# Optimization experiments

Hardware: AMD Instinct MI355X
Metric: run time of the kernel (lower is better)

## Reference

```python
import jax, jax.numpy as jnp
import numpy as np

EPS = 1e-5  # nn.LayerNorm default
T, B, HID, L = 32, 256, 384, 3
E_ENT, E_SPA, E_SCA = 256, 256, 640
D_IN = E_ENT + E_SPA + E_SCA  # 1152


def layer_norm(x, g, b):
    mu = jnp.mean(x, axis=-1, keepdims=True)
    var = jnp.var(x, axis=-1, keepdims=True)
    return (x - mu) * jax.lax.rsqrt(var + EPS) * g + b


def setup_inputs() -> dict:
    key = jax.random.key(0)
    ks = jax.random.split(key, 12)
    s_in = 0.02
    return {
        "embedded_entity": jax.random.normal(ks[0], (T, B, E_ENT), jnp.float32),
        "embedded_spatial": jax.random.normal(ks[1], (T, B, E_SPA), jnp.float32),
        "embedded_scalar": jax.random.normal(ks[2], (T, B, E_SCA), jnp.float32),
        "h0": jnp.zeros((L, B, HID), jnp.float32),
        "c0": jnp.zeros((L, B, HID), jnp.float32),
        "wx0": jax.random.normal(ks[3], (D_IN, 4 * HID), jnp.float32) * s_in,
        "wx1": jax.random.normal(ks[4], (HID, 4 * HID), jnp.float32) * s_in,
        "wx2": jax.random.normal(ks[5], (HID, 4 * HID), jnp.float32) * s_in,
        "wh": jax.random.normal(ks[6], (L, HID, 4 * HID), jnp.float32) * s_in,
        "bias": jnp.zeros((L, 4 * HID), jnp.float32),
        "gxw": jnp.ones((L, 4 * HID), jnp.float32) + 0.01 * jax.random.normal(ks[7], (L, 4 * HID), jnp.float32),
        "gxb": 0.01 * jax.random.normal(ks[8], (L, 4 * HID), jnp.float32),
        "ghw": jnp.ones((L, 4 * HID), jnp.float32) + 0.01 * jax.random.normal(ks[9], (L, 4 * HID), jnp.float32),
        "ghb": 0.01 * jax.random.normal(ks[10], (L, 4 * HID), jnp.float32),
    }


def _ln_lstm(x, h0, c0, wx_list, wh, bias, gxw, gxb, ghw, ghb):
    # x: [T, B, D]; returns output [T, B, H], (H_final, C_final) each [L, B, H]
    Hs, Cs = [], []
    for l in range(wh.shape[0]):
        # LayerNorm is per-row, so the input-side projection+LN can be batched over time
        xg = layer_norm(jnp.einsum('tbd,dk->tbk', x, wx_list[l]), gxw[l], gxb[l])
        wh_l, ghw_l, ghb_l, b_l = wh[l], ghw[l], ghb[l], bias[l]

        def step(carry, xg_t):
            h, c = carry
            gate = xg_t + layer_norm(h @ wh_l, ghw_l, ghb_l) + b_l
            i, f, o, u = jnp.split(gate, 4, axis=-1)
            c = jax.nn.sigmoid(f) * c + jax.nn.sigmoid(i) * jnp.tanh(u)
            h = jax.nn.sigmoid(o) * jnp.tanh(c)
            return (h, c), h

        (h, c), x = jax.lax.scan(step, (h0[l], c0[l]), xg)
        Hs.append(h)
        Cs.append(c)
    return x, jnp.stack(Hs), jnp.stack(Cs)


def reference(embedded_entity, embedded_spatial, embedded_scalar, h0, c0,
              wx0, wx1, wx2, wh, bias, gxw, gxb, ghw, ghb):
    embedded = jnp.concatenate([embedded_entity, embedded_spatial, embedded_scalar], axis=2)
    output, Hn, Cn = _ln_lstm(embedded, h0, c0, [wx0, wx1, wx2], wh, bias, gxw, gxb, ghw, ghb)
    return output, Hn, Cn
```

## Files before the change

### kernel.cpp

```cpp
#include <hip/hip_runtime.h>
#include <math.h>

constexpr int TT = 32;
constexpr int BB = 256;
constexpr int HH = 384;
constexpr int GG = 1536;
constexpr float LN_EPS = 1e-5f;

template<bool CONCAT>
__global__ __launch_bounds__(256)
void gemm64(const float* __restrict__ A,
            const float* __restrict__ Aent, const float* __restrict__ Aspa,
            const float* __restrict__ Asca,
            const float* __restrict__ B, float* __restrict__ C,
            int M, int K, int N)
{
    __shared__ float As[16][64];
    __shared__ float Bs[16][64];
    const int tid = threadIdx.x;
    const int bm = blockIdx.y * 64;
    const int bn = blockIdx.x * 64;
    const int tr = tid >> 4;
    const int tc = tid & 15;
    const int ar = tid >> 2;
    const int ac = (tid & 3) * 4;
    const int br = tid >> 4;
    const int bc = (tid & 15) * 4;

    float acc[4][4] = {};

    for (int k0 = 0; k0 < K; k0 += 16) {
        float4 av;
        const int arow = bm + ar;
        const int acol = k0 + ac;
        if (CONCAT) {
            const float* p;
            if (acol < 256)      p = Aent + arow * 256 + acol;
            else if (acol < 512) p = Aspa + arow * 256 + (acol - 256);
            else                 p = Asca + arow * 640 + (acol - 512);
            av = *reinterpret_cast<const float4*>(p);
        } else {
            av = *reinterpret_cast<const float4*>(A + arow * (long)K + acol);
        }
        As[ac + 0][ar] = av.x;
        As[ac + 1][ar] = av.y;
        As[ac + 2][ar] = av.z;
        As[ac + 3][ar] = av.w;
        *reinterpret_cast<float4*>(&Bs[br][bc]) =
            *reinterpret_cast<const float4*>(B + (k0 + br) * (long)N + bn + bc);
        __syncthreads();
        #pragma unroll
        for (int k = 0; k < 16; ++k) {
            const float4 a = *reinterpret_cast<const float4*>(&As[k][tr * 4]);
            const float4 b = *reinterpret_cast<const float4*>(&Bs[k][tc * 4]);
            acc[0][0] += a.x * b.x; acc[0][1] += a.x * b.y; acc[0][2] += a.x * b.z; acc[0][3] += a.x * b.w;
            acc[1][0] += a.y * b.x; acc[1][1] += a.y * b.y; acc[1][2] += a.y * b.z; acc[1][3] += a.y * b.w;
            acc[2][0] += a.z * b.x; acc[2][1] += a.z * b.y; acc[2][2] += a.z * b.z; acc[2][3] += a.z * b.w;
            acc[3][0] += a.w * b.x; acc[3][1] += a.w * b.y; acc[3][2] += a.w * b.z; acc[3][3] += a.w * b.w;
        }
        __syncthreads();
    }
    #pragma unroll
    for (int i = 0; i < 4; ++i) {
        float4 v = make_float4(acc[i][0], acc[i][1], acc[i][2], acc[i][3]);
        *reinterpret_cast<float4*>(C + (bm + tr * 4 + i) * (long)N + bn + tc * 4) = v;
    }
}

__global__ __launch_bounds__(256)
void ln_rows(float* __restrict__ X, const float* __restrict__ g,
             const float* __restrict__ b)
{
    float* x = X + (long)blockIdx.x * GG;
    const int tid = threadIdx.x;
    float v[6];
    float s = 0.f, q = 0.f;
    #pragma unroll
    for (int i = 0; i < 6; ++i) {
        v[i] = x[tid + i * 256];
        s += v[i];
        q += v[i] * v[i];
    }
    #pragma unroll
    for (int o = 32; o; o >>= 1) {
        s += __shfl_xor(s, o);
        q += __shfl_xor(q, o);
    }
    __shared__ float red[2][4];
    const int wave = tid >> 6;
    if ((tid & 63) == 0) { red[0][wave] = s; red[1][wave] = q; }
    __syncthreads();
    float S = 0.f, Q = 0.f;
    #pragma unroll
    for (int w = 0; w < 4; ++w) { S += red[0][w]; Q += red[1][w]; }
    const float mean = S * (1.0f / GG);
    const float var  = Q * (1.0f / GG) - mean * mean;
    const float rs   = rsqrtf(var + LN_EPS);
    #pragma unroll
    for (int i = 0; i < 6; ++i) {
        const int col = tid + i * 256;
        x[col] = (v[i] - mean) * rs * g[col] + b[col];
    }
}

__device__ __forceinline__ float sigm(float x) { return 1.0f / (1.0f + __expf(-x)); }

__global__ __launch_bounds__(384)
void lstm_cell(const float* __restrict__ tmp,
               const float* __restrict__ xg,
               const float* __restrict__ bias,
               const float* __restrict__ ghw,
               const float* __restrict__ ghb,
               const float* __restrict__ c_in,
               float* __restrict__ h_state,
               float* __restrict__ c_state,
               float* __restrict__ x_out,
               float* __restrict__ hn_out,
               float* __restrict__ cn_out,
               int is_last)
{
    const int b = blockIdx.x;
    const int j = threadIdx.x;
    const float* trow = tmp + (long)b * GG;

    float v[4];
    float s = 0.f, q = 0.f;
    #pragma unroll
    for (int p = 0; p < 4; ++p) {
        v[p] = trow[j + p * HH];
        s += v[p];
        q += v[p] * v[p];
    }
    #pragma unroll
    for (int o = 32; o; o >>= 1) {
        s += __shfl_xor(s, o);
        q += __shfl_xor(q, o);
    }
    __shared__ float red[2][8];
    const int wave = j >> 6;
    if ((j & 63) == 0) { red[0][wave] = s; red[1][wave] = q; }
    __syncthreads();
    float S = 0.f, Q = 0.f;
    #pragma unroll
    for (int w = 0; w < 6; ++w) { S += red[0][w]; Q += red[1][w]; }
    const float mean = S * (1.0f / GG);
    const float var  = Q * (1.0f / GG) - mean * mean;
    const float rs   = rsqrtf(var + LN_EPS);

    const float* xrow = xg + (long)b * GG;
    float gate[4];
    #pragma unroll
    for (int p = 0; p < 4; ++p) {
        const int col = j + p * HH;
        gate[p] = (v[p] - mean) * rs * ghw[col] + ghb[col] + xrow[col] + bias[col];
    }
    const float gi = gate[0], gf = gate[1], go = gate[2], gu = gate[3];
    const float c = sigm(gf) * c_in[(long)b * HH + j] + sigm(gi) * tanhf(gu);
    const float h = sigm(go) * tanhf(c);

    h_state[(long)b * HH + j] = h;
    c_state[(long)b * HH + j] = c;
    x_out[(long)b * HH + j]   = h;
    if (is_last) {
        hn_out[(long)b * HH + j] = h;
        cn_out[(long)b * HH + j] = c;
    }
}

extern "C" void kernel_launch(void* const* d_in, const int* in_sizes, int n_in,
                              void* d_out, int out_size, void* d_ws, size_t ws_size,
                              hipStream_t stream)
{
    const float* ent  = (const float*)d_in[0];
    const float* spa  = (const float*)d_in[1];
    const float* sca  = (const float*)d_in[2];
    const float* h0   = (const float*)d_in[3];
    const float* c0   = (const float*)d_in[4];
    const float* wx[3] = { (const float*)d_in[5], (const float*)d_in[6], (const float*)d_in[7] };
    const float* wh   = (const float*)d_in[8];
    const float* bias = (const float*)d_in[9];
    const float* gxw  = (const float*)d_in[10];
    const float* gxb  = (const float*)d_in[11];
    const float* ghw  = (const float*)d_in[12];
    const float* ghb  = (const float*)d_in[13];

    float* out = (float*)d_out;
    float* out_x  = out;
    float* out_hn = out + (long)TT * BB * HH;
    float* out_cn = out_hn + (long)3 * BB * HH;

    float* ws = (float*)d_ws;
    float* xg      = ws;
    float* xbufA   = xg + (long)TT * BB * GG;
    float* xbufB   = xbufA + (long)TT * BB * HH;
    float* tmp     = xbufB + (long)TT * BB * HH;
    float* h_state = tmp + (long)BB * GG;
    float* c_state = h_state + (long)BB * HH;

    const int M = TT * BB;

    for (int l = 0; l < 3; ++l) {
        const int K = (l == 0) ? 1152 : HH;
        const float* xin = (l == 1) ? xbufA : xbufB;
        float* xout = (l == 0) ? xbufA : (l == 1) ? xbufB : out_x;

        {
            dim3 grid(GG / 64, M / 64);
            if (l == 0)
                gemm64<true><<<grid, 256, 0, stream>>>(nullptr, ent, spa, sca,
                                                       wx[0], xg, M, K, GG);
            else
                gemm64<false><<<grid, 256, 0, stream>>>(xin, nullptr, nullptr, nullptr,
                                                        wx[l], xg, M, K, GG);
        }
        ln_rows<<<M, 256, 0, stream>>>(xg, gxw + l * GG, gxb + l * GG);

        const float* wh_l = wh + (long)l * HH * GG;
        for (int t = 0; t < TT; ++t) {
            const float* h_in = (t == 0) ? (h0 + (long)l * BB * HH) : h_state;
            const float* c_in = (t == 0) ? (c0 + (long)l * BB * HH) : c_state;
            {
                dim3 grid(GG / 64, BB / 64);
                gemm64<false><<<grid, 256, 0, stream>>>(h_in, nullptr, nullptr, nullptr,
                                                        wh_l, tmp, BB, HH, GG);
            }
            lstm_cell<<<BB, 384, 0, stream>>>(
                tmp, xg + (long)t * BB * GG, bias + l * GG,
                ghw + l * GG, ghb + l * GG, c_in,
                h_state, c_state, xout + (long)t * BB * HH,
                out_hn + (long)l * BB * HH, out_cn + (long)l * BB * HH,
                (t == TT - 1) ? 1 : 0);
        }
    }
    (void)in_sizes; (void)n_in; (void)out_size; (void)ws_size;
}
```

Baseline: 3.692 ms.

## Use split-bf16 MFMA GEMMs and a persistent grid-synced LSTM scan kernel

Replaces the FP32 SIMT GEMMs with MFMA bf16 GEMMs that split each FP32 value into three bf16 parts to keep near-FP32 accuracy. Weights are transposed and converted in preprocessing kernels. The 64 per-timestep launches per layer become one persistent 24-block kernel that keeps its recurrent-weight slice in LDS. That kernel computes the LayerNorm statistics through global partial sums and grid-wide atomic barriers, and fuses the cell update. This removes launch overhead and uses matrix cores, but only 24 blocks run the recurrence and each timestep costs several grid barriers.

```diff
diff --git a/kernel.cpp b/kernel.cpp
--- a/kernel.cpp
+++ b/kernel.cpp
@@ -1,69 +1,194 @@
 #include <hip/hip_runtime.h>
 #include <math.h>
 
-constexpr int TT = 32;
-constexpr int BB = 256;
-constexpr int HH = 384;
-constexpr int GG = 1536;
+typedef __bf16 bf16;
+typedef __attribute__((ext_vector_type(8))) __bf16 bf16x8;
+typedef __attribute__((ext_vector_type(4))) float f32x4;
+
+constexpr int TT = 32, BB = 256, HH = 384, GG = 1536;
 constexpr float LN_EPS = 1e-5f;
+constexpr int NBLK = 24;
+
+__device__ __forceinline__ float sigm(float x) { return 1.0f / (1.0f + __expf(-x)); }
+
+__device__ __forceinline__ void split3(float x, bf16& h, bf16& m, bf16& l) {
+    h = (bf16)x; float r = x - (float)h;
+    m = (bf16)r; float r2 = r - (float)m;
+    l = (bf16)r2;
+}
+
+__device__ __forceinline__ void grid_sync(unsigned* bar) {
+    __syncthreads();
+    if (threadIdx.x == 0) {
+        __threadfence();
+        unsigned g = __hip_atomic_load(bar + 1, __ATOMIC_RELAXED, __HIP_MEMORY_SCOPE_AGENT);
+        unsigned old = __hip_atomic_fetch_add(bar + 0, 1u, __ATOMIC_ACQ_REL, __HIP_MEMORY_SCOPE_AGENT);
+        if (old == NBLK - 1) {
+            __hip_atomic_store(bar + 0, 0u, __ATOMIC_RELAXED, __HIP_MEMORY_SCOPE_AGENT);
+            __hip_atomic_fetch_add(bar + 1, 1u, __ATOMIC_ACQ_REL, __HIP_MEMORY_SCOPE_AGENT);
+        } else {
+            while (__hip_atomic_load(bar + 1, __ATOMIC_ACQUIRE, __HIP_MEMORY_SCOPE_AGENT) == g)
+                __builtin_amdgcn_s_sleep(2);
+        }
+        __threadfence();
+    }
+    __syncthreads();
+}
+
+__global__ void init_bar(unsigned* bar) { bar[0] = 0; bar[1] = 0; }
+
+template<bool PERM>
+__global__ __launch_bounds__(256)
+void transpose_cvt3(const float* __restrict__ in, bf16* __restrict__ out,
+                    int K, int N)
+{
+    __shared__ float tile[32][33];
+    const int k0 = blockIdx.y * 32;
+    const int n0 = blockIdx.x * 32;
+    const int tx = threadIdx.x & 31;
+    const int ty = threadIdx.x >> 5;
+    const size_t PS = (size_t)N * K;
+    #pragma unroll
+    for (int i = 0; i < 4; ++i)
+        tile[ty + i * 8][tx] = in[(long)(k0 + ty + i * 8) * N + n0 + tx];
+    __syncthreads();
+    #pragma unroll
+    for (int i = 0; i < 4; ++i) {
+        const int n = n0 + ty + i * 8;
+        int orow;
+        if (PERM) {
+            const int p = n / HH, r = n - p * HH;
+            orow = ((r >> 4) * 4 + p) * 16 + (r & 15);
+        } else orow = n;
+        bf16 h, m, l;
+        split3(tile[tx][ty + i * 8], h, m, l);
+        const size_t base = (size_t)orow * K + k0 + tx;
+        out[base] = h; out[PS + base] = m; out[2 * PS + base] = l;
+    }
+}
 
 template<bool CONCAT>
 __global__ __launch_bounds__(256)
-void gemm64(const float* __restrict__ A,
-            const float* __restrict__ Aent, const float* __restrict__ Aspa,
-            const float* __restrict__ Asca,
-            const float* __restrict__ B, float* __restrict__ C,
-            int M, int K, int N)
+void gemm_proj(const float* __restrict__ A,
+               const float* __restrict__ Aent, const float* __restrict__ Aspa,
+               const float* __restrict__ Asca,
+               const bf16* __restrict__ Bt3, float* __restrict__ C,
+               int K, int N)
 {
-    __shared__ float As[16][64];
-    __shared__ float Bs[16][64];
+    constexpr int LDA = 40;
+    __shared__ bf16 As[3][128 * LDA];
+    __shared__ bf16 Bs[3][128 * LDA];
     const int tid = threadIdx.x;
-    const int bm = blockIdx.y * 64;
-    const int bn = blockIdx.x * 64;
-    const int tr = tid >> 4;
-    const int tc = tid & 15;
-    const int ar = tid >> 2;
-    const int ac = (tid & 3) * 4;
-    const int br = tid >> 4;
-    const int bc = (tid & 15) * 4;
-
-    float acc[4][4] = {};
-
-    for (int k0 = 0; k0 < K; k0 += 16) {
-        float4 av;
-        const int arow = bm + ar;
-        const int acol = k0 + ac;
-        if (CONCAT) {
+    const long bm = (long)blockIdx.y * 128;
+    const int bn = blockIdx.x * 128;
+    const int srow = tid & 127;
+    const int soff = (tid >> 7) * 16;
+    const int lane = tid & 63;
+    const int wid  = tid >> 6;
+    const int wm = (wid >> 1) * 64, wn = (wid & 1) * 64;
+    const int cc = lane & 15, g = lane >> 4;
+    const size_t PS = (size_t)N * K;
+
+    const f32x4 zero = {0.f, 0.f, 0.f, 0.f};
+    f32x4 acc[4][4];
+    #pragma unroll
+    for (int m = 0; m < 4; ++m)
+        #pragma unroll
+        for (int n = 0; n < 4; ++n) acc[m][n] = zero;
+
+    for (int k0 = 0; k0 < K; k0 += 32) {
+        float va[16];
+        if (!CONCAT) {
+            const float* p = A + (bm + srow) * (long)K + k0 + soff;
+            #pragma unroll
+            for (int i = 0; i < 4; ++i) {
+                const float4 v = *(const float4*)(p + i * 4);
+                va[i*4+0] = v.x; va[i*4+1] = v.y; va[i*4+2] = v.z; va[i*4+3] = v.w;
+            }
+        } else {
+            const int acol = k0 + soff;
             const float* p;
-            if (acol < 256)      p = Aent + arow * 256 + acol;
-            else if (acol < 512) p = Aspa + arow * 256 + (acol - 256);
-            else                 p = Asca + arow * 640 + (acol - 512);
-            av = *reinterpret_cast<const float4*>(p);
-        } else {
-            av = *reinterpret_cast<const float4*>(A + arow * (long)K + acol);
-        }
-        As[ac + 0][ar] = av.x;
-        As[ac + 1][ar] = av.y;
-        As[ac + 2][ar] = av.z;
-        As[ac + 3][ar] = av.w;
-        *reinterpret_cast<float4*>(&Bs[br][bc]) =
-            *reinterpret_cast<const float4*>(B + (k0 + br) * (long)N + bn + bc);
+            if (acol < 256)      p = Aent + (bm + srow) * 256 + acol;
+            else if (acol < 512) p = Aspa + (bm + srow) * 256 + (acol - 256);
+            else                 p = Asca + (bm + srow) * 640 + (acol - 512);
+            #pragma unroll
+            for (int i = 0; i < 4; ++i) {
+                const float4 v = *(const float4*)(p + i * 4);
+                va[i*4+0] = v.x; va[i*4+1] = v.y; va[i*4+2] = v.z; va[i*4+3] = v.w;
+            }
+        }
+        bf16 ah[16], am[16], al[16];
+        #pragma unroll
+        for (int e = 0; e < 16; ++e) split3(va[e], ah[e], am[e], al[e]);
+        const bf16* bp = Bt3 + (bn + srow) * (long)K + k0 + soff;
+        const bf16x8 b00 = *(const bf16x8*)bp;
+        const bf16x8 b01 = *(const bf16x8*)(bp + 8);
+        const bf16x8 b10 = *(const bf16x8*)(bp + PS);
+        const bf16x8 b11 = *(const bf16x8*)(bp + PS + 8);
+        const bf16x8 b20 = *(const bf16x8*)(bp + 2 * PS);
+        const bf16x8 b21 = *(const bf16x8*)(bp + 2 * PS + 8);
         __syncthreads();
-        #pragma unroll
-        for (int k = 0; k < 16; ++k) {
-            const float4 a = *reinterpret_cast<const float4*>(&As[k][tr * 4]);
-            const float4 b = *reinterpret_cast<const float4*>(&Bs[k][tc * 4]);
-            acc[0][0] += a.x * b.x; acc[0][1] += a.x * b.y; acc[0][2] += a.x * b.z; acc[0][3] += a.x * b.w;
-            acc[1][0] += a.y * b.x; acc[1][1] += a.y * b.y; acc[1][2] += a.y * b.z; acc[1][3] += a.y * b.w;
-            acc[2][0] += a.z * b.x; acc[2][1] += a.z * b.y; acc[2][2] += a.z * b.z; acc[2][3] += a.z * b.w;
-            acc[3][0] += a.w * b.x; acc[3][1] += a.w * b.y; acc[3][2] += a.w * b.z; acc[3][3] += a.w * b.w;
-        }
+        *(bf16x8*)&As[0][srow * LDA + soff]     = *(bf16x8*)&ah[0];
+        *(bf16x8*)&As[0][srow * LDA + soff + 8] = *(bf16x8*)&ah[8];
+        *(bf16x8*)&As[1][srow * LDA + soff]     = *(bf16x8*)&am[0];
+        *(bf16x8*)&As[1][srow * LDA + soff + 8] = *(bf16x8*)&am[8];
+        *(bf16x8*)&As[2][srow * LDA + soff]     = *(bf16x8*)&al[0];
+        *(bf16x8*)&As[2][srow * LDA + soff + 8] = *(bf16x8*)&al[8];
+        *(bf16x8*)&Bs[0][srow * LDA + soff]     = b00;
+        *(bf16x8*)&Bs[0][srow * LDA + soff + 8] = b01;
+        *(bf16x8*)&Bs[1][srow * LDA + soff]     = b10;
+        *(bf16x8*)&Bs[1][srow * LDA + soff + 8] = b11;
+        *(bf16x8*)&Bs[2][srow * LDA + soff]     = b20;
+        *(bf16x8*)&Bs[2][srow * LDA + soff + 8] = b21;
         __syncthreads();
-    }
-    #pragma unroll
-    for (int i = 0; i < 4; ++i) {
-        float4 v = make_float4(acc[i][0], acc[i][1], acc[i][2], acc[i][3]);
-        *reinterpret_cast<float4*>(C + (bm + tr * 4 + i) * (long)N + bn + tc * 4) = v;
+        bf16x8 a0[4], a1[4], a2[4], bb[4];
+        #pragma unroll
+        for (int m = 0; m < 4; ++m) {
+            const int off = (wm + m * 16 + cc) * LDA + g * 8;
+            a0[m] = *(const bf16x8*)&As[0][off];
+            a1[m] = *(const bf16x8*)&As[1][off];
+            a2[m] = *(const bf16x8*)&As[2][off];
+        }
+        #pragma unroll
+        for (int n = 0; n < 4; ++n)
+            bb[n] = *(const bf16x8*)&Bs[0][(wn + n * 16 + cc) * LDA + g * 8];
+        #pragma unroll
+        for (int m = 0; m < 4; ++m)
+            #pragma unroll
+            for (int n = 0; n < 4; ++n) {
+                acc[m][n] = __builtin_amdgcn_mfma_f32_16x16x32_bf16(a0[m], bb[n], acc[m][n], 0, 0, 0);
+                acc[m][n] = __builtin_amdgcn_mfma_f32_16x16x32_bf16(a1[m], bb[n], acc[m][n], 0, 0, 0);
+                acc[m][n] = __builtin_amdgcn_mfma_f32_16x16x32_bf16(a2[m], bb[n], acc[m][n], 0, 0, 0);
+            }
+        #pragma unroll
+        for (int n = 0; n < 4; ++n)
+            bb[n] = *(const bf16x8*)&Bs[1][(wn + n * 16 + cc) * LDA + g * 8];
+        #pragma unroll
+        for (int m = 0; m < 4; ++m)
+            #pragma unroll
+            for (int n = 0; n < 4; ++n) {
+                acc[m][n] = __builtin_amdgcn_mfma_f32_16x16x32_bf16(a0[m], bb[n], acc[m][n], 0, 0, 0);
+                acc[m][n] = __builtin_amdgcn_mfma_f32_16x16x32_bf16(a1[m], bb[n], acc[m][n], 0, 0, 0);
+            }
+        #pragma unroll
+        for (int n = 0; n < 4; ++n)
+            bb[n] = *(const bf16x8*)&Bs[2][(wn + n * 16 + cc) * LDA + g * 8];
+        #pragma unroll
+        for (int m = 0; m < 4; ++m)
+            #pragma unroll
+            for (int n = 0; n < 4; ++n)
+                acc[m][n] = __builtin_amdgcn_mfma_f32_16x16x32_bf16(a0[m], bb[n], acc[m][n], 0, 0, 0);
+    }
+    #pragma unroll
+    for (int m = 0; m < 4; ++m) {
+        const long row0 = bm + wm + m * 16 + g * 4;
+        #pragma unroll
+        for (int n = 0; n < 4; ++n) {
+            const int col = bn + wn + n * 16 + cc;
+            #pragma unroll
+            for (int r = 0; r < 4; ++r)
+                C[(row0 + r) * (long)N + col] = acc[m][n][r];
+        }
     }
 }
 
@@ -78,14 +203,10 @@
     #pragma unroll
     for (int i = 0; i < 6; ++i) {
         v[i] = x[tid + i * 256];
-        s += v[i];
-        q += v[i] * v[i];
-    }
-    #pragma unroll
-    for (int o = 32; o; o >>= 1) {
-        s += __shfl_xor(s, o);
-        q += __shfl_xor(q, o);
-    }
+        s += v[i]; q += v[i] * v[i];
+    }
+    #pragma unroll
+    for (int o = 32; o; o >>= 1) { s += __shfl_xor(s, o); q += __shfl_xor(q, o); }
     __shared__ float red[2][4];
     const int wave = tid >> 6;
     if ((tid & 63) == 0) { red[0][wave] = s; red[1][wave] = q; }
@@ -103,67 +224,172 @@
     }
 }
 
-__device__ __forceinline__ float sigm(float x) { return 1.0f / (1.0f + __expf(-x)); }
-
-__global__ __launch_bounds__(384)
-void lstm_cell(const float* __restrict__ tmp,
+__device__ __forceinline__ float red16(float v) {
+    v += __shfl_xor(v, 1); v += __shfl_xor(v, 2);
+    v += __shfl_xor(v, 4); v += __shfl_xor(v, 8);
+    return v;
+}
+
+__global__ __launch_bounds__(256)
+void lstm_scan(const bf16* __restrict__ whT3,
                const float* __restrict__ xg,
-               const float* __restrict__ bias,
-               const float* __restrict__ ghw,
-               const float* __restrict__ ghb,
-               const float* __restrict__ c_in,
-               float* __restrict__ h_state,
+               const float* __restrict__ bias_l,
+               const float* __restrict__ ghw_l,
+               const float* __restrict__ ghb_l,
+               const float* __restrict__ h0_l,
+               const float* __restrict__ c0_l,
+               bf16*  __restrict__ hp,
                float* __restrict__ c_state,
-               float* __restrict__ x_out,
-               float* __restrict__ hn_out,
-               float* __restrict__ cn_out,
-               int is_last)
+               float* __restrict__ partials,
+               unsigned* __restrict__ bar,
+               float* __restrict__ xout,
+               float* __restrict__ hn, float* __restrict__ cn)
 {
-    const int b = blockIdx.x;
-    const int j = threadIdx.x;
-    const float* trow = tmp + (long)b * GG;
-
-    float v[4];
-    float s = 0.f, q = 0.f;
+    constexpr int LDB = 392;
+    __shared__ bf16 Bsh[3][64 * LDB];
+    __shared__ float stats[BB][2];
+
+    const int tid = threadIdx.x;
+    const int ni = blockIdx.x;
+    const int mi = tid >> 6;
+    const int lane = tid & 63;
+    const int cc = lane & 15, g = lane >> 4;
+    const size_t SB = (size_t)BB * HH;
+    const size_t WP = (size_t)GG * HH;
+
+    for (int i = ni * 256 + tid; i < BB * HH; i += NBLK * 256) {
+        bf16 h, m, l; split3(h0_l[i], h, m, l);
+        hp[i] = h; hp[SB + i] = m; hp[2 * SB + i] = l;
+        c_state[i] = c0_l[i];
+    }
+    #pragma unroll
+    for (int q = 0; q < 3; ++q) {
+        const bf16* src = whT3 + q * WP + (size_t)ni * 64 * HH;
+        for (int cid = tid; cid < 64 * 48; cid += 256) {
+            const int rl = cid / 48, kc = (cid % 48) * 8;
+            *(bf16x8*)&Bsh[q][rl * LDB + kc] = *(const bf16x8*)(src + rl * HH + kc);
+        }
+    }
+    float gw[4], gc[4];
     #pragma unroll
     for (int p = 0; p < 4; ++p) {
-        v[p] = trow[j + p * HH];
-        s += v[p];
-        q += v[p] * v[p];
-    }
-    #pragma unroll
-    for (int o = 32; o; o >>= 1) {
-        s += __shfl_xor(s, o);
-        q += __shfl_xor(q, o);
-    }
-    __shared__ float red[2][8];
-    const int wave = j >> 6;
-    if ((j & 63) == 0) { red[0][wave] = s; red[1][wave] = q; }
-    __syncthreads();
-    float S = 0.f, Q = 0.f;
-    #pragma unroll
-    for (int w = 0; w < 6; ++w) { S += red[0][w]; Q += red[1][w]; }
-    const float mean = S * (1.0f / GG);
-    const float var  = Q * (1.0f / GG) - mean * mean;
-    const float rs   = rsqrtf(var + LN_EPS);
-
-    const float* xrow = xg + (long)b * GG;
-    float gate[4];
-    #pragma unroll
-    for (int p = 0; p < 4; ++p) {
-        const int col = j + p * HH;
-        gate[p] = (v[p] - mean) * rs * ghw[col] + ghb[col] + xrow[col] + bias[col];
-    }
-    const float gi = gate[0], gf = gate[1], go = gate[2], gu = gate[3];
-    const float c = sigm(gf) * c_in[(long)b * HH + j] + sigm(gi) * tanhf(gu);
-    const float h = sigm(go) * tanhf(c);
-
-    h_state[(long)b * HH + j] = h;
-    c_state[(long)b * HH + j] = c;
-    x_out[(long)b * HH + j]   = h;
-    if (is_last) {
-        hn_out[(long)b * HH + j] = h;
-        cn_out[(long)b * HH + j] = c;
+        const int col = p * HH + ni * 16 + cc;
+        gw[p] = ghw_l[col];
+        gc[p] = ghb_l[col] + bias_l[col];
+    }
+    grid_sync(bar);
+
+    const f32x4 zero = {0.f, 0.f, 0.f, 0.f};
+    for (int t = 0; t < TT; ++t) {
+        f32x4 acc[4][4];
+        #pragma unroll
+        for (int m = 0; m < 4; ++m)
+            #pragma unroll
+            for (int p = 0; p < 4; ++p) acc[m][p] = zero;
+        for (int ks = 0; ks < 12; ++ks) {
+            const int k = ks * 32 + g * 8;
+            bf16x8 a0[4], a1[4], a2[4], bb[4];
+            #pragma unroll
+            for (int m = 0; m < 4; ++m) {
+                const size_t off = (size_t)(mi * 64 + m * 16 + cc) * HH + k;
+                a0[m] = *(const bf16x8*)(hp + off);
+                a1[m] = *(const bf16x8*)(hp + SB + off);
+                a2[m] = *(const bf16x8*)(hp + 2 * SB + off);
+            }
+            #pragma unroll
+            for (int p = 0; p < 4; ++p)
+                bb[p] = *(const bf16x8*)&Bsh[0][(p * 16 + cc) * LDB + k];
+            #pragma unroll
+            for (int m = 0; m < 4; ++m)
+                #pragma unroll
+                for (int p = 0; p < 4; ++p) {
+                    acc[m][p] = __builtin_amdgcn_mfma_f32_16x16x32_bf16(a0[m], bb[p], acc[m][p], 0, 0, 0);
+                    acc[m][p] = __builtin_amdgcn_mfma_f32_16x16x32_bf16(a1[m], bb[p], acc[m][p], 0, 0, 0);
+                    acc[m][p] = __builtin_amdgcn_mfma_f32_16x16x32_bf16(a2[m], bb[p], acc[m][p], 0, 0, 0);
+                }
+            #pragma unroll
+            for (int p = 0; p < 4; ++p)
+                bb[p] = *(const bf16x8*)&Bsh[1][(p * 16 + cc) * LDB + k];
+            #pragma unroll
+            for (int m = 0; m < 4; ++m)
+                #pragma unroll
+                for (int p = 0; p < 4; ++p) {
+                    acc[m][p] = __builtin_amdgcn_mfma_f32_16x16x32_bf16(a0[m], bb[p], acc[m][p], 0, 0, 0);
+                    acc[m][p] = __builtin_amdgcn_mfma_f32_16x16x32_bf16(a1[m], bb[p], acc[m][p], 0, 0, 0);
+                }
+            #pragma unroll
+            for (int p = 0; p < 4; ++p)
+                bb[p] = *(const bf16x8*)&Bsh[2][(p * 16 + cc) * LDB + k];
+            #pragma unroll
+            for (int m = 0; m < 4; ++m)
+                #pragma unroll
+                for (int p = 0; p < 4; ++p)
+                    acc[m][p] = __builtin_amdgcn_mfma_f32_16x16x32_bf16(a0[m], bb[p], acc[m][p], 0, 0, 0);
+        }
+        #pragma unroll
+        for (int m = 0; m < 4; ++m) {
+            float s[4], q[4];
+            #pragma unroll
+            for (int r = 0; r < 4; ++r) { s[r] = 0.f; q[r] = 0.f; }
+            #pragma unroll
+            for (int p = 0; p < 4; ++p)
+                #pragma unroll
+                for (int r = 0; r < 4; ++r) {
+                    const float v = acc[m][p][r];
+                    s[r] += v; q[r] += v * v;
+                }
+            #pragma unroll
+            for (int r = 0; r < 4; ++r) { s[r] = red16(s[r]); q[r] = red16(q[r]); }
+            if (cc == 0) {
+                #pragma unroll
+                for (int r = 0; r < 4; ++r) {
+                    const int row = mi * 64 + m * 16 + g * 4 + r;
+                    partials[(ni * BB + row) * 2 + 0] = s[r];
+                    partials[(ni * BB + row) * 2 + 1] = q[r];
+                }
+            }
+        }
+        grid_sync(bar);
+        {
+            float S = 0.f, Q = 0.f;
+            #pragma unroll
+            for (int n2 = 0; n2 < NBLK; ++n2) {
+                S += partials[(n2 * BB + tid) * 2 + 0];
+                Q += partials[(n2 * BB + tid) * 2 + 1];
+            }
+            const float mean = S * (1.0f / GG);
+            const float var  = Q * (1.0f / GG) - mean * mean;
+            stats[tid][0] = mean;
+            stats[tid][1] = rsqrtf(var + LN_EPS);
+        }
+        __syncthreads();
+        const float* xgt = xg + (long)t * BB * GG;
+        const int j = ni * 16 + cc;
+        #pragma unroll
+        for (int m = 0; m < 4; ++m) {
+            #pragma unroll
+            for (int r = 0; r < 4; ++r) {
+                const int b = mi * 64 + m * 16 + g * 4 + r;
+                const float mean = stats[b][0], rs = stats[b][1];
+                float gate[4];
+                #pragma unroll
+                for (int p = 0; p < 4; ++p) {
+                    const int col = p * HH + ni * 16 + cc;
+                    gate[p] = (acc[m][p][r] - mean) * rs * gw[p] + gc[p]
+                              + xgt[(long)b * GG + col];
+                }
+                const int idx = b * HH + j;
+                const float cprev = c_state[idx];
+                const float cnew  = sigm(gate[1]) * cprev + sigm(gate[0]) * tanhf(gate[3]);
+                const float h     = sigm(gate[2]) * tanhf(cnew);
+                c_state[idx] = cnew;
+                bf16 hh, hm, hl; split3(h, hh, hm, hl);
+                hp[idx] = hh; hp[SB + idx] = hm; hp[2 * SB + idx] = hl;
+                xout[((long)t * BB + b) * HH + j] = h;
+                if (t == TT - 1) { hn[idx] = h; cn[idx] = cnew; }
+            }
+        }
+        grid_sync(bar);
     }
 }
 
@@ -184,53 +410,42 @@
     const float* ghw  = (const float*)d_in[12];
     const float* ghb  = (const float*)d_in[13];
 
-    float* out = (float*)d_out;
+    float* out    = (float*)d_out;
     float* out_x  = out;
     float* out_hn = out + (long)TT * BB * HH;
-    float* out_cn = out_hn + (long)3 * BB * HH;
-
-    float* ws = (float*)d_ws;
-    float* xg      = ws;
-    float* xbufA   = xg + (long)TT * BB * GG;
-    float* xbufB   = xbufA + (long)TT * BB * HH;
-    float* tmp     = xbufB + (long)TT * BB * HH;
-    float* h_state = tmp + (long)BB * GG;
-    float* c_state = h_state + (long)BB * HH;
+    float* out_cn = out_hn + 3L * BB * HH;
+
+    char* w = (char*)d_ws;
+    float* xg      = (float*)w;  w += (size_t)TT * BB * GG * 4;
+    bf16*  wxT3    = (bf16*)w;   w += (size_t)3 * GG * 1152 * 2;
+    bf16*  whT3    = (bf16*)w;   w += (size_t)3 * GG * HH * 2;
+    float* xf      = (float*)w;  w += (size_t)TT * BB * HH * 4;
+    bf16*  hp      = (bf16*)w;   w += (size_t)3 * BB * HH * 2;
+    float* c_state = (float*)w;  w += (size_t)BB * HH * 4;
+    float* parts   = (float*)w;  w += (size_t)NBLK * BB * 2 * 4;
+    unsigned* bar  = (unsigned*)w;
+
+    init_bar<<<1, 1, 0, stream>>>(bar);
 
     const int M = TT * BB;
-
     for (int l = 0; l < 3; ++l) {
         const int K = (l == 0) ? 1152 : HH;
-        const float* xin = (l == 1) ? xbufA : xbufB;
-        float* xout = (l == 0) ? xbufA : (l == 1) ? xbufB : out_x;
-
-        {
-            dim3 grid(GG / 64, M / 64);
-            if (l == 0)
-                gemm64<true><<<grid, 256, 0, stream>>>(nullptr, ent, spa, sca,
-                                                       wx[0], xg, M, K, GG);
-            else
-                gemm64<false><<<grid, 256, 0, stream>>>(xin, nullptr, nullptr, nullptr,
-                                                        wx[l], xg, M, K, GG);
-        }
+        transpose_cvt3<false><<<dim3(GG / 32, K / 32), 256, 0, stream>>>(wx[l], wxT3, K, GG);
+        transpose_cvt3<true ><<<dim3(GG / 32, HH / 32), 256, 0, stream>>>(wh + (long)l * HH * GG, whT3, HH, GG);
+
+        dim3 pgrid(GG / 128, M / 128);
+        if (l == 0)
+            gemm_proj<true ><<<pgrid, 256, 0, stream>>>(nullptr, ent, spa, sca, wxT3, xg, K, GG);
+        else
+            gemm_proj<false><<<pgrid, 256, 0, stream>>>(xf, nullptr, nullptr, nullptr, wxT3, xg, K, GG);
         ln_rows<<<M, 256, 0, stream>>>(xg, gxw + l * GG, gxb + l * GG);
 
-        const float* wh_l = wh + (long)l * HH * GG;
-        for (int t = 0; t < TT; ++t) {
-            const float* h_in = (t == 0) ? (h0 + (long)l * BB * HH) : h_state;
-            const float* c_in = (t == 0) ? (c0 + (long)l * BB * HH) : c_state;
-            {
-                dim3 grid(GG / 64, BB / 64);
-                gemm64<false><<<grid, 256, 0, stream>>>(h_in, nullptr, nullptr, nullptr,
-                                                        wh_l, tmp, BB, HH, GG);
-            }
-            lstm_cell<<<BB, 384, 0, stream>>>(
-                tmp, xg + (long)t * BB * GG, bias + l * GG,
-                ghw + l * GG, ghb + l * GG, c_in,
-                h_state, c_state, xout + (long)t * BB * HH,
-                out_hn + (long)l * BB * HH, out_cn + (long)l * BB * HH,
-                (t == TT - 1) ? 1 : 0);
-        }
+        lstm_scan<<<NBLK, 256, 0, stream>>>(whT3, xg,
+            bias + l * GG, ghw + l * GG, ghb + l * GG,
+            h0 + (long)l * BB * HH, c0 + (long)l * BB * HH,
+            hp, c_state, parts, bar,
+            (l == 2) ? out_x : xf,
+            out_hn + (long)l * BB * HH, out_cn + (long)l * BB * HH);
     }
     (void)in_sizes; (void)n_in; (void)out_size; (void)ws_size;
 }
```

Result: slower. 5.471 ms (+48.2%).
